# Optimization experiments

Hardware: AMD Instinct MI355X
Metric: run time of the kernel (lower is better)

The kernel has to match this reference:

```python
import jax, jax.numpy as jnp
import numpy as np

K = 0.1  # curvature (called k in the module)
EPS = 1e-15

def setup_inputs() -> dict:
    key = jax.random.key(0)
    k1, k2, k3 = jax.random.split(key, 3)
    B, C, D = 2048, 1000, 64
    x = jax.random.normal(k1, (B, D), dtype=jnp.float32) * 0.05  # inside ball
    a_vals = jax.random.normal(k2, (C, D), dtype=jnp.float32) * 0.05
    p_vals = jax.random.normal(k3, (C, D), dtype=jnp.float32) * 0.05
    return {"x": x, "a_vals": a_vals, "p_vals": p_vals}

def reference(x, a_vals, p_vals):
    k = jnp.asarray(K, dtype=x.dtype)
    sqrt_k = jnp.sqrt(k)
    # poincare_exp0: exponential map at the origin
    p_norm = jnp.maximum(jnp.linalg.norm(p_vals, axis=1, keepdims=True), EPS)  # [C,1]
    p_poin = jnp.tanh(sqrt_k * p_norm) * p_vals / (sqrt_k * p_norm)            # [C,D]
    # conformal scaling of a (as written in the module: 1 + k*||p||^2)
    p2 = jnp.sum(p_poin * p_poin, axis=1)                                      # [C]
    a_poin = a_vals * (1.0 + k * p2)[:, None]                                  # [C,D]
    # hyperbolic softmax logits
    lam = 2.0 / (1.0 - k * p2)                                                 # [C]
    a_norm = jnp.maximum(jnp.linalg.norm(a_poin, axis=1), EPS)                 # [C]
    scale = lam * a_norm / sqrt_k                                              # [C]
    # mobius addition of (-p) (+) x, batched -> [C,B,D]
    mp = -p_poin                                                               # [C,D]
    xy = jnp.einsum('cd,bd->cb', mp, x)                                        # [C,B]
    x2 = jnp.sum(mp * mp, axis=-1)[:, None]                                    # [C,1]
    y2 = jnp.sum(x * x, axis=-1)[None, :]                                      # [1,B]
    num = ((1.0 + 2.0 * k * xy + k * y2)[..., None] * mp[:, None, :]
           + (1.0 - k * x2)[..., None] * x[None, :, :])                        # [C,B,D]
    den = 1.0 + 2.0 * k * xy + (k * k) * x2 * y2                               # [C,B]
    mob = num / den[..., None]                                                 # [C,B,D]
    numer = 2.0 * sqrt_k * jnp.einsum('cbd,cd->cb', mob, a_poin)               # [C,B]
    denom = a_norm[:, None] * (1.0 - k * jnp.sum(mob * mob, axis=-1))          # [C,B]
    logits = scale[:, None] * jnp.arcsinh(numer / denom)                       # [C,B]
    return logits.T                                                            # [B,C]
```

## Files before the change

kernel.cpp:

```cpp
#include <hip/hip_runtime.h>
#include <hip/hip_bf16.h>
#include <math.h>

#define KCURV  0.1f
#define SQRT_K 0.31622776601683794f
#define INV_SQRT_K 3.1622776601683795f
#define TD 64
#define BM 64
#define BN 64
#define LDK 72

typedef __bf16  bf16x8  __attribute__((ext_vector_type(8)));
typedef float   f32x4   __attribute__((ext_vector_type(4)));

__device__ __forceinline__ unsigned short f2bf(float f) {
    __hip_bfloat16 h = __float2bfloat16(f);
    return *(unsigned short*)&h;
}

__global__ __launch_bounds__(256) void hyper_mlr_kernel(
    const float* __restrict__ x,
    const float* __restrict__ a_vals,
    const float* __restrict__ p_vals,
    float* __restrict__ out,
    int B, int C)
{
    __shared__ unsigned short Xb[BM][LDK];
    __shared__ unsigned short Pb[BN][LDK];
    __shared__ unsigned short Ab[BN][LDK];
    __shared__ float x2s[BN], pas[BN], ans[BN], scs[BN], y2s[BM];

    const int tid = threadIdx.x;
    const int cb = blockIdx.x * BN;
    const int rb = blockIdx.y * BM;

    {
        int row = tid >> 2, q = tid & 3;
        int gr = rb + row; if (gr >= B) gr = B - 1;
        const float* xr = x + (size_t)gr * TD + q * 16;
        float v[16];
        #pragma unroll
        for (int m = 0; m < 4; ++m)
            *(float4*)&v[m * 4] = *(const float4*)(xr + m * 4);
        float s = 0.f;
        #pragma unroll
        for (int u = 0; u < 16; ++u) s = fmaf(v[u], v[u], s);
        s += __shfl_xor(s, 1, 64);
        s += __shfl_xor(s, 2, 64);
        if (q == 0) y2s[row] = s;
        unsigned short ub[16];
        #pragma unroll
        for (int u = 0; u < 16; ++u) ub[u] = f2bf(v[u]);
        *(ulonglong2*)&Xb[row][q * 16]     = *(const ulonglong2*)&ub[0];
        *(ulonglong2*)&Xb[row][q * 16 + 8] = *(const ulonglong2*)&ub[8];
    }

    {
        int c = tid >> 2, q = tid & 3;
        int gc = cb + c; if (gc >= C) gc = C - 1;
        const float* pr = p_vals + (size_t)gc * TD + q * 16;
        const float* ar = a_vals + (size_t)gc * TD + q * 16;
        float pv[16], av[16];
        #pragma unroll
        for (int m = 0; m < 4; ++m) {
            *(float4*)&pv[m * 4] = *(const float4*)(pr + m * 4);
            *(float4*)&av[m * 4] = *(const float4*)(ar + m * 4);
        }
        float s_pp = 0.f, s_aa = 0.f;
        #pragma unroll
        for (int u = 0; u < 16; ++u) {
            s_pp = fmaf(pv[u], pv[u], s_pp);
            s_aa = fmaf(av[u], av[u], s_aa);
        }
        s_pp += __shfl_xor(s_pp, 1, 64); s_pp += __shfl_xor(s_pp, 2, 64);
        s_aa += __shfl_xor(s_aa, 1, 64); s_aa += __shfl_xor(s_aa, 2, 64);

        float pn = sqrtf(s_pp); if (pn < 1e-15f) pn = 1e-15f;
        float arg = SQRT_K * pn;
        float t = tanhf(arg);
        float factor = t / arg;
        float p2 = factor * factor * s_pp;
        float ca = 1.0f + KCURV * p2;
        float anorm = ca * sqrtf(s_aa); if (anorm < 1e-15f) anorm = 1e-15f;
        float lam = 2.0f / (1.0f - KCURV * p2);
        float scale = lam * anorm * INV_SQRT_K;

        float s_pa = 0.f;
        #pragma unroll
        for (int u = 0; u < 16; ++u) s_pa = fmaf(pv[u], av[u], s_pa);
        s_pa += __shfl_xor(s_pa, 1, 64); s_pa += __shfl_xor(s_pa, 2, 64);
        float pa = -factor * ca * s_pa;

        if (q == 0) { x2s[c] = p2; pas[c] = pa; ans[c] = anorm; scs[c] = scale; }

        unsigned short ubp[16], uba[16];
        #pragma unroll
        for (int u = 0; u < 16; ++u) {
            ubp[u] = f2bf(-factor * pv[u]);
            uba[u] = f2bf(ca * av[u]);
        }
        *(ulonglong2*)&Pb[c][q * 16]     = *(const ulonglong2*)&ubp[0];
        *(ulonglong2*)&Pb[c][q * 16 + 8] = *(const ulonglong2*)&ubp[8];
        *(ulonglong2*)&Ab[c][q * 16]     = *(const ulonglong2*)&uba[0];
        *(ulonglong2*)&Ab[c][q * 16 + 8] = *(const ulonglong2*)&uba[8];
    }
    __syncthreads();

    const int w    = tid >> 6;
    const int lane = tid & 63;
    const int m16  = lane & 15;
    const int quad = lane >> 4;

    f32x4 accP[4], accA[4];
    #pragma unroll
    for (int t = 0; t < 4; ++t) {
        accP[t] = (f32x4){0.f, 0.f, 0.f, 0.f};
        accA[t] = (f32x4){0.f, 0.f, 0.f, 0.f};
    }

    #pragma unroll
    for (int step = 0; step < 2; ++step) {
        const int ko = quad * 8 + step * 32;
        bf16x8 af = *(const bf16x8*)&Xb[16 * w + m16][ko];
        #pragma unroll
        for (int t = 0; t < 4; ++t) {
            bf16x8 bp = *(const bf16x8*)&Pb[16 * t + m16][ko];
            bf16x8 ba = *(const bf16x8*)&Ab[16 * t + m16][ko];
            accP[t] = __builtin_amdgcn_mfma_f32_16x16x32_bf16(af, bp, accP[t], 0, 0, 0);
            accA[t] = __builtin_amdgcn_mfma_f32_16x16x32_bf16(af, ba, accA[t], 0, 0, 0);
        }
    }

    #pragma unroll
    for (int t = 0; t < 4; ++t) {
        const int cl = 16 * t + m16;
        const int gc = cb + cl;
        const float x2 = x2s[cl], pa = pas[cl], an = ans[cl], sc = scs[cl];
        const float beta = 1.0f - KCURV * x2;
        #pragma unroll
        for (int r = 0; r < 4; ++r) {
            const int rl = 16 * w + quad * 4 + r;
            const int gr = rb + rl;
            const float y2 = y2s[rl];
            const float xy = accP[t][r];
            const float xa = accA[t][r];
            float alpha = 1.0f + 2.0f * KCURV * xy + KCURV * y2;
            float den = 1.0f + 2.0f * KCURV * xy + (KCURV * KCURV) * x2 * y2;
            float rden = 1.0f / den;
            float numer = 2.0f * SQRT_K * (alpha * pa + beta * xa) * rden;
            float mob2 = (alpha * alpha * x2 + 2.0f * alpha * beta * xy
                          + beta * beta * y2) * (rden * rden);
            float denom = an * (1.0f - KCURV * mob2);
            float lg = sc * asinhf(numer / denom);
            if (gr < B && gc < C) out[(size_t)gr * C + gc] = lg;
        }
    }
}

extern "C" void kernel_launch(void* const* d_in, const int* in_sizes, int n_in,
                              void* d_out, int out_size, void* d_ws, size_t ws_size,
                              hipStream_t stream) {
    const float* x      = (const float*)d_in[0];
    const float* a_vals = (const float*)d_in[1];
    const float* p_vals = (const float*)d_in[2];
    int B = in_sizes[0] / TD;
    int C = in_sizes[1] / TD;
    dim3 grid((C + BN - 1) / BN, (B + BM - 1) / BM);
    hyper_mlr_kernel<<<grid, dim3(256), 0, stream>>>(
        x, a_vals, p_vals, (float*)d_out, B, C);
}
```

Baseline: 73.26 us.

## Split into prep kernel and GEMM kernel; simplify epilogue math with fast intrinsics

Preprocessing (bf16 conversion, norms, per-class scalars) moves out of the GEMM kernel into a separate prep kernel that writes to workspace. Each x row and class row is now prepared once instead of being recomputed by every tile that uses it. The GEMM kernel loads its MFMA fragments straight from global memory into registers with no LDS or barrier. The epilogue is also rewritten algebraically to use one reciprocal plus fast log/rcp intrinsics instead of asinhf and divides. In exchange it adds a second launch and a workspace round trip, and the fast intrinsics are less accurate.

```diff
diff --git a/kernel.cpp b/kernel.cpp
--- a/kernel.cpp
+++ b/kernel.cpp
@@ -3,12 +3,11 @@
 #include <math.h>
 
 #define KCURV  0.1f
+#define KK     0.010000001f
 #define SQRT_K 0.31622776601683794f
+#define TWO_SQRT_K 0.6324555320336759f
 #define INV_SQRT_K 3.1622776601683795f
 #define TD 64
-#define BM 64
-#define BN 64
-#define LDK 72
 
 typedef __bf16  bf16x8  __attribute__((ext_vector_type(8)));
 typedef float   f32x4   __attribute__((ext_vector_type(4)));
@@ -18,25 +17,22 @@
     return *(unsigned short*)&h;
 }
 
-__global__ __launch_bounds__(256) void hyper_mlr_kernel(
-    const float* __restrict__ x,
-    const float* __restrict__ a_vals,
+__global__ __launch_bounds__(256) void prep_kernel(
+    const float* __restrict__ x, const float* __restrict__ a_vals,
     const float* __restrict__ p_vals,
-    float* __restrict__ out,
-    int B, int C)
+    unsigned short* __restrict__ Xbf, unsigned short* __restrict__ Pbf,
+    unsigned short* __restrict__ Abf,
+    float* __restrict__ y2g, float* __restrict__ x2g, float* __restrict__ pag,
+    float* __restrict__ ang, float* __restrict__ scg,
+    int B, int C, int rowBlocks)
 {
-    __shared__ unsigned short Xb[BM][LDK];
-    __shared__ unsigned short Pb[BN][LDK];
-    __shared__ unsigned short Ab[BN][LDK];
-    __shared__ float x2s[BN], pas[BN], ans[BN], scs[BN], y2s[BM];
-
     const int tid = threadIdx.x;
-    const int cb = blockIdx.x * BN;
-    const int rb = blockIdx.y * BM;
-
-    {
-        int row = tid >> 2, q = tid & 3;
-        int gr = rb + row; if (gr >= B) gr = B - 1;
+    const int item = (blockIdx.x < rowBlocks ? blockIdx.x
+                                             : blockIdx.x - rowBlocks) * 64 + (tid >> 2);
+    const int q = tid & 3;
+
+    if (blockIdx.x < rowBlocks) {
+        int gr = item < B ? item : B - 1;
         const float* xr = x + (size_t)gr * TD + q * 16;
         float v[16];
         #pragma unroll
@@ -47,17 +43,15 @@
         for (int u = 0; u < 16; ++u) s = fmaf(v[u], v[u], s);
         s += __shfl_xor(s, 1, 64);
         s += __shfl_xor(s, 2, 64);
-        if (q == 0) y2s[row] = s;
+        if (q == 0) y2g[item] = s;
         unsigned short ub[16];
         #pragma unroll
         for (int u = 0; u < 16; ++u) ub[u] = f2bf(v[u]);
-        *(ulonglong2*)&Xb[row][q * 16]     = *(const ulonglong2*)&ub[0];
-        *(ulonglong2*)&Xb[row][q * 16 + 8] = *(const ulonglong2*)&ub[8];
-    }
-
-    {
-        int c = tid >> 2, q = tid & 3;
-        int gc = cb + c; if (gc >= C) gc = C - 1;
+        unsigned short* dst = Xbf + (size_t)item * TD + q * 16;
+        *(ulonglong2*)dst       = *(const ulonglong2*)&ub[0];
+        *(ulonglong2*)(dst + 8) = *(const ulonglong2*)&ub[8];
+    } else {
+        int gc = item < C ? item : C - 1;
         const float* pr = p_vals + (size_t)gc * TD + q * 16;
         const float* ar = a_vals + (size_t)gc * TD + q * 16;
         float pv[16], av[16];
@@ -66,14 +60,16 @@
             *(float4*)&pv[m * 4] = *(const float4*)(pr + m * 4);
             *(float4*)&av[m * 4] = *(const float4*)(ar + m * 4);
         }
-        float s_pp = 0.f, s_aa = 0.f;
+        float s_pp = 0.f, s_aa = 0.f, s_pa = 0.f;
         #pragma unroll
         for (int u = 0; u < 16; ++u) {
             s_pp = fmaf(pv[u], pv[u], s_pp);
             s_aa = fmaf(av[u], av[u], s_aa);
+            s_pa = fmaf(pv[u], av[u], s_pa);
         }
         s_pp += __shfl_xor(s_pp, 1, 64); s_pp += __shfl_xor(s_pp, 2, 64);
         s_aa += __shfl_xor(s_aa, 1, 64); s_aa += __shfl_xor(s_aa, 2, 64);
+        s_pa += __shfl_xor(s_pa, 1, 64); s_pa += __shfl_xor(s_pa, 2, 64);
 
         float pn = sqrtf(s_pp); if (pn < 1e-15f) pn = 1e-15f;
         float arg = SQRT_K * pn;
@@ -84,32 +80,55 @@
         float anorm = ca * sqrtf(s_aa); if (anorm < 1e-15f) anorm = 1e-15f;
         float lam = 2.0f / (1.0f - KCURV * p2);
         float scale = lam * anorm * INV_SQRT_K;
-
-        float s_pa = 0.f;
-        #pragma unroll
-        for (int u = 0; u < 16; ++u) s_pa = fmaf(pv[u], av[u], s_pa);
-        s_pa += __shfl_xor(s_pa, 1, 64); s_pa += __shfl_xor(s_pa, 2, 64);
         float pa = -factor * ca * s_pa;
 
-        if (q == 0) { x2s[c] = p2; pas[c] = pa; ans[c] = anorm; scs[c] = scale; }
-
+        if (q == 0) {
+            x2g[item] = p2; pag[item] = pa; ang[item] = anorm; scg[item] = scale;
+        }
         unsigned short ubp[16], uba[16];
         #pragma unroll
         for (int u = 0; u < 16; ++u) {
             ubp[u] = f2bf(-factor * pv[u]);
             uba[u] = f2bf(ca * av[u]);
         }
-        *(ulonglong2*)&Pb[c][q * 16]     = *(const ulonglong2*)&ubp[0];
-        *(ulonglong2*)&Pb[c][q * 16 + 8] = *(const ulonglong2*)&ubp[8];
-        *(ulonglong2*)&Ab[c][q * 16]     = *(const ulonglong2*)&uba[0];
-        *(ulonglong2*)&Ab[c][q * 16 + 8] = *(const ulonglong2*)&uba[8];
-    }
-    __syncthreads();
-
+        unsigned short* dp = Pbf + (size_t)item * TD + q * 16;
+        unsigned short* da = Abf + (size_t)item * TD + q * 16;
+        *(ulonglong2*)dp       = *(const ulonglong2*)&ubp[0];
+        *(ulonglong2*)(dp + 8) = *(const ulonglong2*)&ubp[8];
+        *(ulonglong2*)da       = *(const ulonglong2*)&uba[0];
+        *(ulonglong2*)(da + 8) = *(const ulonglong2*)&uba[8];
+    }
+}
+
+__global__ __launch_bounds__(256) void mlr_gemm_kernel(
+    const unsigned short* __restrict__ Xbf, const unsigned short* __restrict__ Pbf,
+    const unsigned short* __restrict__ Abf,
+    const float* __restrict__ y2g, const float* __restrict__ x2g,
+    const float* __restrict__ pag, const float* __restrict__ ang,
+    const float* __restrict__ scg,
+    float* __restrict__ out, int B, int C)
+{
+    const int tid  = threadIdx.x;
     const int w    = tid >> 6;
     const int lane = tid & 63;
     const int m16  = lane & 15;
     const int quad = lane >> 4;
+    const int cb   = blockIdx.x * 64;
+    const int rb   = blockIdx.y * 64;
+    const int arow = rb + 16 * w + m16;
+
+    bf16x8 af[2], bp[4][2], ba[4][2];
+    #pragma unroll
+    for (int step = 0; step < 2; ++step) {
+        const int ko = quad * 8 + step * 32;
+        af[step] = *(const bf16x8*)(Xbf + (size_t)arow * TD + ko);
+        #pragma unroll
+        for (int t = 0; t < 4; ++t) {
+            const size_t crow = (size_t)(cb + 16 * t + m16) * TD + ko;
+            bp[t][step] = *(const bf16x8*)(Pbf + crow);
+            ba[t][step] = *(const bf16x8*)(Abf + crow);
+        }
+    }
 
     f32x4 accP[4], accA[4];
     #pragma unroll
@@ -117,42 +136,40 @@
         accP[t] = (f32x4){0.f, 0.f, 0.f, 0.f};
         accA[t] = (f32x4){0.f, 0.f, 0.f, 0.f};
     }
-
     #pragma unroll
     for (int step = 0; step < 2; ++step) {
-        const int ko = quad * 8 + step * 32;
-        bf16x8 af = *(const bf16x8*)&Xb[16 * w + m16][ko];
         #pragma unroll
         for (int t = 0; t < 4; ++t) {
-            bf16x8 bp = *(const bf16x8*)&Pb[16 * t + m16][ko];
-            bf16x8 ba = *(const bf16x8*)&Ab[16 * t + m16][ko];
-            accP[t] = __builtin_amdgcn_mfma_f32_16x16x32_bf16(af, bp, accP[t], 0, 0, 0);
-            accA[t] = __builtin_amdgcn_mfma_f32_16x16x32_bf16(af, ba, accA[t], 0, 0, 0);
-        }
-    }
+            accP[t] = __builtin_amdgcn_mfma_f32_16x16x32_bf16(af[step], bp[t][step], accP[t], 0, 0, 0);
+            accA[t] = __builtin_amdgcn_mfma_f32_16x16x32_bf16(af[step], ba[t][step], accA[t], 0, 0, 0);
+        }
+    }
+
+    const float4 y2v = *(const float4*)(y2g + rb + 16 * w + quad * 4);
+    const float* y2p = (const float*)&y2v;
 
     #pragma unroll
     for (int t = 0; t < 4; ++t) {
-        const int cl = 16 * t + m16;
-        const int gc = cb + cl;
-        const float x2 = x2s[cl], pa = pas[cl], an = ans[cl], sc = scs[cl];
+        const int cl = cb + 16 * t + m16;
+        const float x2 = x2g[cl], pa = pag[cl], an = ang[cl], sc = scg[cl];
         const float beta = 1.0f - KCURV * x2;
+        const float kkx2 = KK * x2;
         #pragma unroll
         for (int r = 0; r < 4; ++r) {
-            const int rl = 16 * w + quad * 4 + r;
-            const int gr = rb + rl;
-            const float y2 = y2s[rl];
+            const int gr = rb + 16 * w + quad * 4 + r;
+            const float y2 = y2p[r];
             const float xy = accP[t][r];
             const float xa = accA[t][r];
-            float alpha = 1.0f + 2.0f * KCURV * xy + KCURV * y2;
-            float den = 1.0f + 2.0f * KCURV * xy + (KCURV * KCURV) * x2 * y2;
-            float rden = 1.0f / den;
-            float numer = 2.0f * SQRT_K * (alpha * pa + beta * xa) * rden;
-            float mob2 = (alpha * alpha * x2 + 2.0f * alpha * beta * xy
-                          + beta * beta * y2) * (rden * rden);
-            float denom = an * (1.0f - KCURV * mob2);
-            float lg = sc * asinhf(numer / denom);
-            if (gr < B && gc < C) out[(size_t)gr * C + gc] = lg;
+            float t1    = fmaf(2.0f * KCURV, xy, 1.0f);
+            float den   = fmaf(kkx2, y2, t1);
+            float alpha = fmaf(KCURV, y2, t1);
+            float g     = fmaf(alpha, pa, beta * xa);
+            float M     = fmaf(alpha * alpha, x2,
+                          fmaf(2.0f * alpha * beta, xy, beta * beta * y2));
+            float dd    = fmaf(den, den, -KCURV * M);
+            float z     = TWO_SQRT_K * g * den * __builtin_amdgcn_rcpf(an * dd);
+            float lg    = sc * __logf(z + sqrtf(fmaf(z, z, 1.0f)));
+            if (cl < C) out[(size_t)gr * C + cl] = lg;
         }
     }
 }
@@ -163,9 +180,26 @@
     const float* x      = (const float*)d_in[0];
     const float* a_vals = (const float*)d_in[1];
     const float* p_vals = (const float*)d_in[2];
-    int B = in_sizes[0] / TD;
-    int C = in_sizes[1] / TD;
-    dim3 grid((C + BN - 1) / BN, (B + BM - 1) / BM);
-    hyper_mlr_kernel<<<grid, dim3(256), 0, stream>>>(
-        x, a_vals, p_vals, (float*)d_out, B, C);
-}
+    const int B = in_sizes[0] / TD;
+    const int C = in_sizes[1] / TD;
+    const int rowBlocks = (B + 63) / 64;
+    const int clsBlocks = (C + 63) / 64;
+    const int CPAD = clsBlocks * 64;
+
+    char* ws = (char*)d_ws;
+    unsigned short* Xbf = (unsigned short*)ws;
+    unsigned short* Pbf = (unsigned short*)(ws + (size_t)B * TD * 2);
+    unsigned short* Abf = (unsigned short*)(ws + (size_t)B * TD * 2 + (size_t)CPAD * TD * 2);
+    float* y2g = (float*)(ws + (size_t)B * TD * 2 + (size_t)CPAD * TD * 4);
+    float* x2g = y2g + B;
+    float* pag = x2g + CPAD;
+    float* ang = pag + CPAD;
+    float* scg = ang + CPAD;
+
+    prep_kernel<<<rowBlocks + clsBlocks, 256, 0, stream>>>(
+        x, a_vals, p_vals, Xbf, Pbf, Abf, y2g, x2g, pag, ang, scg, B, C, rowBlocks);
+
+    dim3 grid(clsBlocks, rowBlocks);
+    mlr_gemm_kernel<<<grid, dim3(256), 0, stream>>>(
+        Xbf, Pbf, Abf, y2g, x2g, pag, ang, scg, (float*)d_out, B, C);
+}
```

Result: faster. 69.44 us (-5.2%).
